# Kernel optimization log

Hardware: AMD Instinct MI355X
Metric: run time of the kernel (lower is better)

## Reference

```python
import jax, jax.numpy as jnp
import numpy as np

EPS = 1e-5

def _dwconv1d(x, w):
    # x: [B,C,L], w: [C,k] depthwise kernel, same padding, no bias
    k = w.shape[1]
    return jax.lax.conv_general_dilated(
        x, w[:, None, :], window_strides=(1,), padding=[(k // 2, k // 2)],
        dimension_numbers=('NCH', 'OIH', 'NCH'), feature_group_count=x.shape[1])

def _bn1d(x, gamma, beta, mean, var):
    # eval-mode BatchNorm over channel dim of [B,C,L]
    scale = gamma / jnp.sqrt(var + EPS)
    return (x - mean[:, None]) * scale[:, None] + beta[:, None]

def _strip_pool(x, w3, w7, gamma, beta, mean, var):
    # mean of [identity, dwconv_k3, dwconv_k7] then BN
    out = (x + _dwconv1d(x, w3) + _dwconv1d(x, w7)) / 3.0
    return _bn1d(out, gamma, beta, mean, var)

def _hswish(x):
    return x * jnp.clip(x + 3.0, 0.0, 6.0) / 6.0

def setup_inputs() -> dict:
    key = jax.random.key(0)
    ks = jax.random.split(key, 8)
    B, C, H, W = 32, 256, 64, 64   # C = 2*inp
    MIP = 8                        # max(8, 128//32)
    O = 256                        # 2*oup
    f32 = jnp.float32
    x = jax.random.normal(ks[0], (B, C, H, W), f32)
    def bn_params(k, n):
        k1, k2 = jax.random.split(k)
        return (1.0 + 0.1 * jax.random.normal(k1, (n,), f32),      # gamma
                0.1 * jax.random.normal(k2, (n,), f32),            # beta
                jnp.zeros((n,), f32),                              # running_mean
                jnp.ones((n,), f32))                               # running_var
    sph_g, sph_b, sph_m, sph_v = bn_params(ks[1], C)
    spw_g, spw_b, spw_m, spw_v = bn_params(ks[2], C)
    bn1_g, bn1_b, bn1_m, bn1_v = bn_params(ks[3], MIP)
    s = 0.1
    return {
        'x': x,
        'sph_w3': s * jax.random.normal(ks[4], (C, 3), f32),
        'sph_w7': s * jax.random.normal(ks[4], (C, 7), f32),
        'sph_gamma': sph_g, 'sph_beta': sph_b, 'sph_mean': sph_m, 'sph_var': sph_v,
        'spw_w3': s * jax.random.normal(ks[5], (C, 3), f32),
        'spw_w7': s * jax.random.normal(ks[5], (C, 7), f32),
        'spw_gamma': spw_g, 'spw_beta': spw_b, 'spw_mean': spw_m, 'spw_var': spw_v,
        'conv1_w': s * jax.random.normal(ks[6], (MIP, C), f32),
        'bn1_gamma': bn1_g, 'bn1_beta': bn1_b, 'bn1_mean': bn1_m, 'bn1_var': bn1_v,
        'convh_w': s * jax.random.normal(ks[7], (O, MIP), f32),
        'convw_w': s * jax.random.normal(ks[7], (O, MIP), f32),
    }

def reference(x, sph_w3, sph_w7, sph_gamma, sph_beta, sph_mean, sph_var,
              spw_w3, spw_w7, spw_gamma, spw_beta, spw_mean, spw_var,
              conv1_w, bn1_gamma, bn1_beta, bn1_mean, bn1_var,
              convh_w, convw_w):
    B, C, H, W = x.shape
    # coordinate pooling -> strips [B,C,H] and [B,C,W]
    x_h = jnp.mean(x, axis=3)
    x_w = jnp.mean(x, axis=2)
    # multi-scale strip pooling
    x_h = _strip_pool(x_h, sph_w3, sph_w7, sph_gamma, sph_beta, sph_mean, sph_var)
    x_w = _strip_pool(x_w, spw_w3, spw_w7, spw_gamma, spw_beta, spw_mean, spw_var)
    # shared 1x1 conv + BN + h_swish on concatenated strip [B,C,H+W]
    y = jnp.concatenate([x_h, x_w], axis=2)
    y = jnp.einsum('mc,bcl->bml', conv1_w, y)
    y = _bn1d(y, bn1_gamma, bn1_beta, bn1_mean, bn1_var)
    y = _hswish(y)
    y_h, y_w = y[:, :, :H], y[:, :, H:]
    # per-direction gates [B,O,H] / [B,O,W]
    a_h = jax.nn.sigmoid(jnp.einsum('om,bmh->boh', convh_w, y_h))
    a_w = jax.nn.sigmoid(jnp.einsum('om,bmw->bow', convw_w, y_w))
    return x * a_h[:, :, :, None] * a_w[:, :, None, :]
```

## Files before the change

kernel.cpp:

```cpp
#include <hip/hip_runtime.h>
#include <math.h>

#define EPSF 1e-5f

__global__ __launch_bounds__(256) void k1_pool_strip(
    const float* __restrict__ x,
    const float* __restrict__ sph_w3, const float* __restrict__ sph_w7,
    const float* __restrict__ sph_g,  const float* __restrict__ sph_b,
    const float* __restrict__ sph_m,  const float* __restrict__ sph_v,
    const float* __restrict__ spw_w3, const float* __restrict__ spw_w7,
    const float* __restrict__ spw_g,  const float* __restrict__ spw_b,
    const float* __restrict__ spw_m,  const float* __restrict__ spw_v,
    float* __restrict__ sp)
{
    __shared__ __align__(16) float tile[64][68];
    __shared__ __align__(16) float rpart[256];
    __shared__ float cpart[4][64];
    __shared__ float mh[64];
    __shared__ float mw[64];

    const int plane = blockIdx.x;
    const int c = plane & 255;
    const float* xp = x + (size_t)plane * 4096;
    const int t = threadIdx.x;
    const int r = t >> 2, q = t & 3;

    const float4* src = (const float4*)(xp + r * 64 + q * 16);
    float4 v0 = src[0], v1 = src[1], v2 = src[2], v3 = src[3];
    float4* dst = (float4*)&tile[r][q * 16];
    dst[0] = v0; dst[1] = v1; dst[2] = v2; dst[3] = v3;
    rpart[t] = (v0.x + v0.y + v0.z + v0.w) + (v1.x + v1.y + v1.z + v1.w)
             + (v2.x + v2.y + v2.z + v2.w) + (v3.x + v3.y + v3.z + v3.w);
    __syncthreads();

    {
        const int cc = t & 63, qw = t >> 6;
        float s = 0.f;
        #pragma unroll
        for (int i = 0; i < 16; ++i) s += tile[qw * 16 + i][cc];
        cpart[qw][cc] = s;
    }
    __syncthreads();

    if (t < 64) {
        float4 rp = ((const float4*)rpart)[t];
        mh[t] = (rp.x + rp.y + rp.z + rp.w) * (1.f / 64.f);
        mw[t] = (cpart[0][t] + cpart[1][t] + cpart[2][t] + cpart[3][t]) * (1.f / 64.f);
    }
    __syncthreads();

    if (t < 128) {
        const int l = t & 63;
        const bool is_h = (t < 64);
        const float* m  = is_h ? mh     : mw;
        const float* w3 = is_h ? sph_w3 : spw_w3;
        const float* w7 = is_h ? sph_w7 : spw_w7;
        const float* g  = is_h ? sph_g  : spw_g;
        const float* bb = is_h ? sph_b  : spw_b;
        const float* mu = is_h ? sph_m  : spw_m;
        const float* vv = is_h ? sph_v  : spw_v;

        float v[7];
        #pragma unroll
        for (int j = 0; j < 7; ++j) {
            int idx = l - 3 + j;
            v[j] = (idx >= 0 && idx < 64) ? m[idx] : 0.f;
        }
        float c3 = w3[c*3+0]*v[2] + w3[c*3+1]*v[3] + w3[c*3+2]*v[4];
        float c7 = 0.f;
        #pragma unroll
        for (int j = 0; j < 7; ++j) c7 += w7[c*7+j]*v[j];

        float o = (v[3] + c3 + c7) * (1.f / 3.f);
        float scale = g[c] * rsqrtf(vv[c] + EPSF);
        o = (o - mu[c]) * scale + bb[c];
        sp[(size_t)plane * 128 + (is_h ? l : 64 + l)] = o;
    }
}

__global__ __launch_bounds__(256) void k2_mid(
    const float* __restrict__ sp,
    const float* __restrict__ conv1_w,
    const float* __restrict__ bn1_g, const float* __restrict__ bn1_b,
    const float* __restrict__ bn1_m, const float* __restrict__ bn1_v,
    const float* __restrict__ convh_w, const float* __restrict__ convw_w,
    float* __restrict__ a_h, float* __restrict__ a_w)
{
    __shared__ float spc[256 * 16];
    __shared__ float w1t[256 * 8];
    __shared__ float wos[256 * 8];
    __shared__ float ys[8 * 16];

    const int b  = blockIdx.x >> 3;
    const int lc = blockIdx.x & 7;
    const int l0 = lc * 16;
    const bool is_h = (l0 < 64);
    const int t = threadIdx.x;

    const float* spb = sp + (size_t)b * 256 * 128;
    const float* wo  = is_h ? convh_w : convw_w;

    for (int j = t; j < 4096; j += 256) {
        int cc = j >> 4, li = j & 15;
        spc[j] = spb[cc * 128 + l0 + li];
    }
    for (int j = t; j < 2048; j += 256) {
        int cc = j >> 3, m = j & 7;
        w1t[j] = conv1_w[m * 256 + cc];
        wos[j] = wo[j];
    }
    __syncthreads();

    if (t < 128) {
        const int m = t >> 4, li = t & 15;
        float acc = 0.f;
        for (int cc = 0; cc < 256; ++cc)
            acc += w1t[cc * 8 + m] * spc[cc * 16 + li];
        float scale = bn1_g[m] * rsqrtf(bn1_v[m] + EPSF);
        float val = (acc - bn1_m[m]) * scale + bn1_b[m];
        val = val * fminf(fmaxf(val + 3.f, 0.f), 6.f) * (1.f / 6.f);
        ys[m * 16 + li] = val;
    }
    __syncthreads();

    float* ab = (is_h ? a_h : a_w) + (size_t)b * 256 * 64;
    const int pos0 = is_h ? l0 : l0 - 64;
    const int li = t & 15, ob = t >> 4;
    #pragma unroll
    for (int i = 0; i < 16; ++i) {
        const int o = i * 16 + ob;
        float s = 0.f;
        #pragma unroll
        for (int m = 0; m < 8; ++m)
            s += wos[o * 8 + m] * ys[m * 16 + li];
        ab[o * 64 + pos0 + li] = 1.f / (1.f + __expf(-s));
    }
}

__global__ __launch_bounds__(256) void k3_apply(
    const float* __restrict__ x,
    const float* __restrict__ a_h, const float* __restrict__ a_w,
    float* __restrict__ out)
{
    const size_t g = (size_t)blockIdx.x * 256 + threadIdx.x;
    float4 xv = ((const float4*)x)[g];
    const size_t idx = g * 4;
    const int w0 = (int)(idx & 63);
    const int h  = (int)((idx >> 6) & 63);
    const size_t bc = idx >> 12;
    const float ah = a_h[bc * 64 + h];
    const float4 aw = *(const float4*)(a_w + bc * 64 + w0);
    float4 o;
    o.x = xv.x * ah * aw.x;
    o.y = xv.y * ah * aw.y;
    o.z = xv.z * ah * aw.z;
    o.w = xv.w * ah * aw.w;
    ((float4*)out)[g] = o;
}

extern "C" void kernel_launch(void* const* d_in, const int* in_sizes, int n_in,
                              void* d_out, int out_size, void* d_ws, size_t ws_size,
                              hipStream_t stream) {
    const float* x       = (const float*)d_in[0];
    const float* sph_w3  = (const float*)d_in[1];
    const float* sph_w7  = (const float*)d_in[2];
    const float* sph_g   = (const float*)d_in[3];
    const float* sph_b   = (const float*)d_in[4];
    const float* sph_m   = (const float*)d_in[5];
    const float* sph_v   = (const float*)d_in[6];
    const float* spw_w3  = (const float*)d_in[7];
    const float* spw_w7  = (const float*)d_in[8];
    const float* spw_g   = (const float*)d_in[9];
    const float* spw_b   = (const float*)d_in[10];
    const float* spw_m   = (const float*)d_in[11];
    const float* spw_v   = (const float*)d_in[12];
    const float* conv1_w = (const float*)d_in[13];
    const float* bn1_g   = (const float*)d_in[14];
    const float* bn1_b   = (const float*)d_in[15];
    const float* bn1_m   = (const float*)d_in[16];
    const float* bn1_v   = (const float*)d_in[17];
    const float* convh_w = (const float*)d_in[18];
    const float* convw_w = (const float*)d_in[19];

    float* ws  = (float*)d_ws;
    float* sp  = ws;
    float* a_h = ws + 1048576;
    float* a_w = ws + 1048576 + 524288;

    const int B = 32, C = 256;

    k1_pool_strip<<<B * C, 256, 0, stream>>>(
        x, sph_w3, sph_w7, sph_g, sph_b, sph_m, sph_v,
        spw_w3, spw_w7, spw_g, spw_b, spw_m, spw_v, sp);

    k2_mid<<<B * 8, 256, 0, stream>>>(
        sp, conv1_w, bn1_g, bn1_b, bn1_m, bn1_v, convh_w, convw_w, a_h, a_w);

    k3_apply<<<32768, 256, 0, stream>>>(x, a_h, a_w, (float*)d_out);
}
```

Before: 292.0 us.

## Fuse gate projection and sigmoid into per-plane apply kernel

The middle kernel now writes only the small post-hswish y tensor. The O×MIP gate projection and sigmoid move into the apply kernel, which now runs one block per (b,c) plane. Each block computes its 128 gate values into shared memory and then scales the 64×64 plane with float4 loads and stores. This drops the a_h/a_w round trip through global memory and the per-element gate gathers, at the cost of a barrier and a small per-block compute prologue before the stores.

```diff
diff --git a/kernel.cpp b/kernel.cpp
--- a/kernel.cpp
+++ b/kernel.cpp
@@ -78,27 +78,22 @@
     }
 }
 
-__global__ __launch_bounds__(256) void k2_mid(
+__global__ __launch_bounds__(256) void k2_y(
     const float* __restrict__ sp,
     const float* __restrict__ conv1_w,
     const float* __restrict__ bn1_g, const float* __restrict__ bn1_b,
     const float* __restrict__ bn1_m, const float* __restrict__ bn1_v,
-    const float* __restrict__ convh_w, const float* __restrict__ convw_w,
-    float* __restrict__ a_h, float* __restrict__ a_w)
+    float* __restrict__ y)
 {
     __shared__ float spc[256 * 16];
     __shared__ float w1t[256 * 8];
-    __shared__ float wos[256 * 8];
-    __shared__ float ys[8 * 16];
 
     const int b  = blockIdx.x >> 3;
     const int lc = blockIdx.x & 7;
     const int l0 = lc * 16;
-    const bool is_h = (l0 < 64);
     const int t = threadIdx.x;
 
     const float* spb = sp + (size_t)b * 256 * 128;
-    const float* wo  = is_h ? convh_w : convw_w;
 
     for (int j = t; j < 4096; j += 256) {
         int cc = j >> 4, li = j & 15;
@@ -107,7 +102,6 @@
     for (int j = t; j < 2048; j += 256) {
         int cc = j >> 3, m = j & 7;
         w1t[j] = conv1_w[m * 256 + cc];
-        wos[j] = wo[j];
     }
     __syncthreads();
 
@@ -119,43 +113,55 @@
         float scale = bn1_g[m] * rsqrtf(bn1_v[m] + EPSF);
         float val = (acc - bn1_m[m]) * scale + bn1_b[m];
         val = val * fminf(fmaxf(val + 3.f, 0.f), 6.f) * (1.f / 6.f);
-        ys[m * 16 + li] = val;
-    }
-    __syncthreads();
-
-    float* ab = (is_h ? a_h : a_w) + (size_t)b * 256 * 64;
-    const int pos0 = is_h ? l0 : l0 - 64;
-    const int li = t & 15, ob = t >> 4;
-    #pragma unroll
-    for (int i = 0; i < 16; ++i) {
-        const int o = i * 16 + ob;
-        float s = 0.f;
-        #pragma unroll
-        for (int m = 0; m < 8; ++m)
-            s += wos[o * 8 + m] * ys[m * 16 + li];
-        ab[o * 64 + pos0 + li] = 1.f / (1.f + __expf(-s));
+        y[b * 1024 + m * 128 + l0 + li] = val;
     }
 }
 
 __global__ __launch_bounds__(256) void k3_apply(
     const float* __restrict__ x,
-    const float* __restrict__ a_h, const float* __restrict__ a_w,
+    const float* __restrict__ y,
+    const float* __restrict__ convh_w, const float* __restrict__ convw_w,
     float* __restrict__ out)
 {
-    const size_t g = (size_t)blockIdx.x * 256 + threadIdx.x;
-    float4 xv = ((const float4*)x)[g];
-    const size_t idx = g * 4;
-    const int w0 = (int)(idx & 63);
-    const int h  = (int)((idx >> 6) & 63);
-    const size_t bc = idx >> 12;
-    const float ah = a_h[bc * 64 + h];
-    const float4 aw = *(const float4*)(a_w + bc * 64 + w0);
-    float4 o;
-    o.x = xv.x * ah * aw.x;
-    o.y = xv.y * ah * aw.y;
-    o.z = xv.z * ah * aw.z;
-    o.w = xv.w * ah * aw.w;
-    ((float4*)out)[g] = o;
+    __shared__ __align__(16) float a_sh[128];
+
+    const int plane = blockIdx.x;
+    const int b = plane >> 8, c = plane & 255;
+    const int t = threadIdx.x;
+    const int r = t >> 2, q = t & 3;
+
+    const float4* src = (const float4*)(x + (size_t)plane * 4096 + r * 64 + q * 16);
+    float4 v0 = src[0], v1 = src[1], v2 = src[2], v3 = src[3];
+
+    if (t < 128) {
+        const bool is_h = (t < 64);
+        const int pos = t & 63;
+        const float* w  = (is_h ? convh_w : convw_w) + c * 8;
+        const float* yb = y + b * 1024 + (is_h ? 0 : 64) + pos;
+        float s = 0.f;
+        #pragma unroll
+        for (int m = 0; m < 8; ++m) s += w[m] * yb[m * 128];
+        a_sh[t] = 1.f / (1.f + __expf(-s));
+    }
+    __syncthreads();
+
+    const float ah = a_sh[r];
+    const float4 aw0 = ((const float4*)&a_sh[64])[q * 4 + 0];
+    const float4 aw1 = ((const float4*)&a_sh[64])[q * 4 + 1];
+    const float4 aw2 = ((const float4*)&a_sh[64])[q * 4 + 2];
+    const float4 aw3 = ((const float4*)&a_sh[64])[q * 4 + 3];
+
+    float4* dst = (float4*)(out + (size_t)plane * 4096 + r * 64 + q * 16);
+    float4 o0, o1, o2, o3;
+    o0.x = v0.x * ah * aw0.x; o0.y = v0.y * ah * aw0.y;
+    o0.z = v0.z * ah * aw0.z; o0.w = v0.w * ah * aw0.w;
+    o1.x = v1.x * ah * aw1.x; o1.y = v1.y * ah * aw1.y;
+    o1.z = v1.z * ah * aw1.z; o1.w = v1.w * ah * aw1.w;
+    o2.x = v2.x * ah * aw2.x; o2.y = v2.y * ah * aw2.y;
+    o2.z = v2.z * ah * aw2.z; o2.w = v2.w * ah * aw2.w;
+    o3.x = v3.x * ah * aw3.x; o3.y = v3.y * ah * aw3.y;
+    o3.z = v3.z * ah * aw3.z; o3.w = v3.w * ah * aw3.w;
+    dst[0] = o0; dst[1] = o1; dst[2] = o2; dst[3] = o3;
 }
 
 extern "C" void kernel_launch(void* const* d_in, const int* in_sizes, int n_in,
@@ -184,8 +190,7 @@
 
     float* ws  = (float*)d_ws;
     float* sp  = ws;
-    float* a_h = ws + 1048576;
-    float* a_w = ws + 1048576 + 524288;
+    float* yw  = ws + 1048576;
 
     const int B = 32, C = 256;
 
@@ -193,8 +198,8 @@
         x, sph_w3, sph_w7, sph_g, sph_b, sph_m, sph_v,
         spw_w3, spw_w7, spw_g, spw_b, spw_m, spw_v, sp);
 
-    k2_mid<<<B * 8, 256, 0, stream>>>(
-        sp, conv1_w, bn1_g, bn1_b, bn1_m, bn1_v, convh_w, convw_w, a_h, a_w);
-
-    k3_apply<<<32768, 256, 0, stream>>>(x, a_h, a_w, (float*)d_out);
-}
+    k2_y<<<B * 8, 256, 0, stream>>>(
+        sp, conv1_w, bn1_g, bn1_b, bn1_m, bn1_v, yw);
+
+    k3_apply<<<B * C, 256, 0, stream>>>(x, yw, convh_w, convw_w, (float*)d_out);
+}
```

New measurement: 297.6 us. About the same (+1.9%).
